# Performance work log

Hardware: AMD Instinct MI355X
Metric: run time of the kernel (lower is better)

Reference implementation:

```python
import jax, jax.numpy as jnp
import numpy as np

N, E, IN, ED, H, C, G, NC = 50000, 800000, 128, 32, 4, 16, 64, 2
HC = H * C  # 64
NEG_SLOPE = 0.2
EPS = 1e-5


def _layernorm(x, g, b):
    mu = jnp.mean(x, axis=-1, keepdims=True)
    var = jnp.mean((x - mu) ** 2, axis=-1, keepdims=True)
    return (x - mu) * jax.lax.rsqrt(var + EPS) * g + b


def _gat(x, src, dst, edge_attr, W, a_src, a_dst, We, a_edge, b):
    """PyG GATConv (v1) with edge features, concat=True."""
    n = x.shape[0]
    h, c = a_src.shape
    xw = (x @ W).reshape(n, h, c)                       # [N,H,C]
    al_src = jnp.sum(xw * a_src, axis=-1)               # [N,H]
    al_dst = jnp.sum(xw * a_dst, axis=-1)               # [N,H]
    ew = (edge_attr @ We).reshape(-1, h, c)             # [Ef,H,C]
    al_e = jnp.sum(ew * a_edge, axis=-1)                # [Ef,H]
    alpha = al_src[src] + al_dst[dst] + al_e            # [Ef,H]
    alpha = jnp.where(alpha > 0, alpha, NEG_SLOPE * alpha)
    # segment softmax over incoming edges of each dst node
    amax = jax.ops.segment_max(alpha, dst, num_segments=n)
    amax = jnp.where(jnp.isfinite(amax), amax, 0.0)
    ex = jnp.exp(alpha - amax[dst])
    denom = jax.ops.segment_sum(ex, dst, num_segments=n)
    att = ex / (denom[dst] + 1e-16)                     # [Ef,H]
    msg = xw[src] * att[:, :, None]                     # [Ef,H,C]
    out = jax.ops.segment_sum(msg, dst, num_segments=n) # [N,H,C]
    return out.reshape(n, h * c) + b


def setup_inputs() -> dict:
    ks = jax.random.split(jax.random.key(0), 24)
    s = 0.1
    inp = {
        "x": jax.random.normal(ks[0], (N, IN), jnp.float32),
        "edge_attr": jax.random.normal(ks[1], (E, ED), jnp.float32),
        "W1": jax.random.normal(ks[2], (IN, HC), jnp.float32) * s,
        "as1": jax.random.normal(ks[3], (H, C), jnp.float32) * s,
        "ad1": jax.random.normal(ks[4], (H, C), jnp.float32) * s,
        "We1": jax.random.normal(ks[5], (ED, HC), jnp.float32) * s,
        "ae1": jax.random.normal(ks[6], (H, C), jnp.float32) * s,
        "b1": jnp.zeros((HC,), jnp.float32),
        "W2": jax.random.normal(ks[7], (HC, HC), jnp.float32) * s,
        "as2": jax.random.normal(ks[8], (H, C), jnp.float32) * s,
        "ad2": jax.random.normal(ks[9], (H, C), jnp.float32) * s,
        "We2": jax.random.normal(ks[10], (ED, HC), jnp.float32) * s,
        "ae2": jax.random.normal(ks[11], (H, C), jnp.float32) * s,
        "b2": jnp.zeros((HC,), jnp.float32),
        "g1": jnp.ones((HC,), jnp.float32),
        "be1": jnp.zeros((HC,), jnp.float32),
        "fw1": jax.random.normal(ks[12], (HC, 32), jnp.float32) * s,
        "fb1": jnp.zeros((32,), jnp.float32),
        "g2": jnp.ones((32,), jnp.float32),
        "be2": jnp.zeros((32,), jnp.float32),
        "fw2": jax.random.normal(ks[13], (32, NC), jnp.float32) * s,
        "fb2": jnp.zeros((NC,), jnp.float32),
        "edge_index": jax.random.randint(ks[14], (2, E), 0, N, jnp.int64),
        "batch": jnp.sort(jax.random.randint(ks[15], (N,), 0, G, jnp.int64)),
    }
    return inp


def reference(x, edge_attr, W1, as1, ad1, We1, ae1, b1, W2, as2, ad2, We2, ae2,
              b2, g1, be1, fw1, fb1, g2, be2, fw2, fb2, edge_index, batch):
    src, dst = edge_index[0], edge_index[1]
    e = edge_attr.shape[0]
    # add_self_loops with fill_value='mean' (mean of incoming edge_attr per node)
    cnt = jax.ops.segment_sum(jnp.ones((e,), x.dtype), dst, num_segments=N)
    loop_ea = jax.ops.segment_sum(edge_attr, dst, num_segments=N) / jnp.clip(cnt, 1.0)[:, None]
    ar = jnp.arange(N)
    src_f = jnp.concatenate([src, ar])
    dst_f = jnp.concatenate([dst, ar])
    ea_f = jnp.concatenate([edge_attr, loop_ea], axis=0)

    h = _gat(x, src_f, dst_f, ea_f, W1, as1, ad1, We1, ae1, b1)
    h = jax.nn.relu(h)
    h = _layernorm(h, g1, be1)
    h = _gat(h, src_f, dst_f, ea_f, W2, as2, ad2, We2, ae2, b2)
    h = jax.nn.relu(h)
    pooled = jax.ops.segment_max(h, batch, num_segments=G)   # global_max_pool
    pooled = jnp.where(jnp.isfinite(pooled), pooled, 0.0)
    z = pooled @ fw1 + fb1
    z = _layernorm(z, g2, be2)
    z = jax.nn.relu(z)
    # dropout(p=0.4) is identity in eval mode
    z = z @ fw2 + fb2
    return jax.nn.log_softmax(z, axis=1)
```

## Files before the change

kernel.cpp:

```cpp
#include <hip/hip_runtime.h>
#include <math.h>

#define N_NODES 50000
#define N_EDGES 800000
#define IN_DIM 128
#define ED_DIM 32
#define NH 4
#define CH 16
#define HC 64
#define NG 64
#define NCL 2
#define NEG_SLOPE 0.2f
#define LN_EPS 1e-5f
#define NBLK1 196

__global__ void k_hist(const int* __restrict__ dst, int* __restrict__ cnt,
                       int* __restrict__ rank_e) {
    int e = blockIdx.x * 256 + threadIdx.x;
    if (e < N_EDGES) rank_e[e] = atomicAdd(&cnt[dst[e]], 1);
}

__global__ void k_scan_local(const int* __restrict__ cnt, int* __restrict__ tmp_ex,
                             int* __restrict__ bsum) {
    __shared__ int sd[256];
    int t = threadIdx.x, idx = blockIdx.x * 256 + t;
    int v = (idx < N_NODES) ? cnt[idx] : 0;
    sd[t] = v; __syncthreads();
    for (int off = 1; off < 256; off <<= 1) {
        int add = (t >= off) ? sd[t - off] : 0;
        __syncthreads();
        sd[t] += add;
        __syncthreads();
    }
    if (idx < N_NODES) tmp_ex[idx] = sd[t] - v;
    if (t == 255) bsum[blockIdx.x] = sd[t];
}

__global__ void k_scan_final(const int* __restrict__ tmp_ex, const int* __restrict__ bsum,
                             int* __restrict__ row_start) {
    __shared__ int sd[256];
    int t = threadIdx.x;
    int v = (t < NBLK1) ? bsum[t] : 0;
    sd[t] = v; __syncthreads();
    for (int off = 1; off < 256; off <<= 1) {
        int add = (t >= off) ? sd[t - off] : 0;
        __syncthreads();
        sd[t] += add;
        __syncthreads();
    }
    int boff = sd[blockIdx.x] - bsum[blockIdx.x];
    int idx = blockIdx.x * 256 + t;
    if (idx < N_NODES) row_start[idx] = tmp_ex[idx] + boff;
    if (idx == 0) row_start[N_NODES] = N_EDGES;
}

__global__ void k_edge_fused(const float* __restrict__ ea,
                             const float* __restrict__ We1, const float* __restrict__ ae1,
                             const float* __restrict__ We2, const float* __restrict__ ae2,
                             const int* __restrict__ dstI, const int* __restrict__ srcI,
                             const int* __restrict__ rank_e, const int* __restrict__ row_start,
                             float4* __restrict__ ale1, float4* __restrict__ ale2,
                             int* __restrict__ src_csr) {
    __shared__ float sVe[ED_DIM * 8];
    int t = threadIdx.x;
    {
        int d = t >> 3, k = t & 7;
        int l = k >> 2, h = k & 3;
        const float* We = l ? We2 : We1;
        const float* ae = l ? ae2 : ae1;
        float s = 0.f;
        #pragma unroll
        for (int c = 0; c < CH; ++c) s += We[d * HC + h * CH + c] * ae[h * CH + c];
        sVe[d * 8 + k] = s;
    }
    __syncthreads();
    int e = blockIdx.x * 256 + t;
    if (e >= N_EDGES) return;
    float a[8];
    #pragma unroll
    for (int k = 0; k < 8; ++k) a[k] = 0.f;
    const float4* er4 = (const float4*)(ea + (long long)e * ED_DIM);
    #pragma unroll
    for (int q = 0; q < ED_DIM / 4; ++q) {
        float4 v = er4[q];
        float ev[4] = {v.x, v.y, v.z, v.w};
        #pragma unroll
        for (int u = 0; u < 4; ++u) {
            #pragma unroll
            for (int k = 0; k < 8; ++k) a[k] += ev[u] * sVe[(q * 4 + u) * 8 + k];
        }
    }
    int pos = row_start[dstI[e]] + rank_e[e];
    src_csr[pos] = srcI[e];
    ale1[pos] = make_float4(a[0], a[1], a[2], a[3]);
    ale2[pos] = make_float4(a[4], a[5], a[6], a[7]);
}

template<int K>
__global__ void k_xw(const float* __restrict__ X, const float* __restrict__ W,
                     const float* __restrict__ AS, const float* __restrict__ AD,
                     float* __restrict__ XW, float* __restrict__ ALS, float* __restrict__ ALD) {
    __shared__ float sW[K * HC];
    __shared__ float sX[16 * K];
    int t = threadIdx.x;
    for (int i = t; i < K * HC; i += 256) sW[i] = W[i];
    int nb = blockIdx.x * 16;
    for (int i = t; i < 16 * K; i += 256) sX[i] = X[(long long)nb * K + i];
    __syncthreads();
    int sub = t >> 6, j = t & 63;
    float acc[4] = {0.f, 0.f, 0.f, 0.f};
    #pragma unroll 8
    for (int k = 0; k < K; ++k) {
        float wv = sW[k * HC + j];
        #pragma unroll
        for (int q = 0; q < 4; ++q) acc[q] += sX[(sub + 4 * q) * K + k] * wv;
    }
    float as_ = AS[j], ad_ = AD[j];
    #pragma unroll
    for (int q = 0; q < 4; ++q) {
        int n = nb + sub + 4 * q;
        XW[(long long)n * HC + j] = acc[q];
        float vs = acc[q] * as_, vd = acc[q] * ad_;
        #pragma unroll
        for (int m = 1; m < 16; m <<= 1) { vs += __shfl_xor(vs, m); vd += __shfl_xor(vd, m); }
        if ((j & 15) == 0) {
            int h = j >> 4;
            ALS[n * 4 + h] = vs; ALD[n * 4 + h] = vd;
        }
    }
}

template<bool DO_LN>
__global__ void k_agg(const int* __restrict__ rs, const int* __restrict__ srcs,
                      const float* __restrict__ ale,
                      const float* __restrict__ ALS, const float* __restrict__ ALD,
                      const float* __restrict__ XW, const float* __restrict__ bias,
                      const float* __restrict__ gam, const float* __restrict__ bet,
                      float* __restrict__ OUT) {
    int n = (blockIdx.x * blockDim.x + threadIdx.x) >> 6;
    if (n >= N_NODES) return;
    int lane = threadIdx.x & 63;
    int h = lane >> 4;
    int e0 = rs[n], e1 = rs[n + 1];
    float adn = ALD[n * 4 + h];
    float acc0 = 0.f, l0 = 0.f, as0 = 0.f;
    float acc1 = 0.f, l1 = 0.f, as1 = 0.f;
    float acc2 = 0.f, l2 = 0.f, as2 = 0.f;
    float acc3 = 0.f, l3 = 0.f, as3 = 0.f;
    int e = e0;
    for (; e + 3 < e1; e += 4) {
        int sA = srcs[e], sB = srcs[e + 1], sC = srcs[e + 2], sD = srcs[e + 3];
        float aeA = ale[(e) * 4 + h];
        float aeB = ale[(e + 1) * 4 + h];
        float aeC = ale[(e + 2) * 4 + h];
        float aeD = ale[(e + 3) * 4 + h];
        float xA = XW[sA * HC + lane];
        float xB = XW[sB * HC + lane];
        float xC = XW[sC * HC + lane];
        float xD = XW[sD * HC + lane];
        float aA = ALS[sA * 4 + h] + adn + aeA;
        float aB = ALS[sB * 4 + h] + adn + aeB;
        float aC = ALS[sC * 4 + h] + adn + aeC;
        float aD = ALS[sD * 4 + h] + adn + aeD;
        aA = aA > 0.f ? aA : NEG_SLOPE * aA;
        aB = aB > 0.f ? aB : NEG_SLOPE * aB;
        aC = aC > 0.f ? aC : NEG_SLOPE * aC;
        aD = aD > 0.f ? aD : NEG_SLOPE * aD;
        float qA = __expf(aA), qB = __expf(aB), qC = __expf(aC), qD = __expf(aD);
        acc0 += qA * xA; l0 += qA; as0 += aeA;
        acc1 += qB * xB; l1 += qB; as1 += aeB;
        acc2 += qC * xC; l2 += qC; as2 += aeC;
        acc3 += qD * xD; l3 += qD; as3 += aeD;
    }
    for (; e < e1; ++e) {
        int sA = srcs[e];
        float aeA = ale[(e) * 4 + h];
        float xA = XW[sA * HC + lane];
        float aA = ALS[sA * 4 + h] + adn + aeA;
        aA = aA > 0.f ? aA : NEG_SLOPE * aA;
        float qA = __expf(aA);
        acc0 += qA * xA; l0 += qA; as0 += aeA;
    }
    int d = e1 - e0;
    float invd = 1.f / (float)(d > 0 ? d : 1);
    float aSelf = ALS[n * 4 + h] + adn + (as0 + as1 + as2 + as3) * invd;
    aSelf = aSelf > 0.f ? aSelf : NEG_SLOPE * aSelf;
    float pS = __expf(aSelf);
    float acc = (acc0 + acc1) + (acc2 + acc3) + pS * XW[n * HC + lane];
    float l = (l0 + l1) + (l2 + l3) + pS;
    float v = acc / (l + 1e-16f) + bias[lane];
    v = fmaxf(v, 0.f);
    if (DO_LN) {
        float s1 = v;
        #pragma unroll
        for (int mm = 1; mm < 64; mm <<= 1) s1 += __shfl_xor(s1, mm);
        float mean = s1 * (1.f / 64.f);
        float dd = v - mean;
        float s2 = dd * dd;
        #pragma unroll
        for (int mm = 1; mm < 64; mm <<= 1) s2 += __shfl_xor(s2, mm);
        float var = s2 * (1.f / 64.f);
        v = dd * rsqrtf(var + LN_EPS) * gam[lane] + bet[lane];
    }
    OUT[(long long)n * HC + lane] = v;
}

__global__ void k_pool(const float* __restrict__ H2, const int* __restrict__ batch,
                       float* __restrict__ pooled) {
    int j = threadIdx.x & 63;
    int r = threadIdx.x >> 6;
    int base = blockIdx.x * 128;
    int gcur = -1; float rm = 0.f;
    for (int n = base + r; n < base + 128 && n < N_NODES; n += 4) {
        int g = batch[n];
        if (g != gcur) {
            if (gcur >= 0) atomicMax((unsigned int*)&pooled[gcur * HC + j], __float_as_uint(rm));
            gcur = g; rm = 0.f;
        }
        rm = fmaxf(rm, H2[(long long)n * HC + j]);
    }
    if (gcur >= 0) atomicMax((unsigned int*)&pooled[gcur * HC + j], __float_as_uint(rm));
}

__global__ void k_head(const float* __restrict__ pooled,
                       const float* __restrict__ fw1, const float* __restrict__ fb1,
                       const float* __restrict__ g2, const float* __restrict__ be2,
                       const float* __restrict__ fw2, const float* __restrict__ fb2,
                       float* __restrict__ out) {
    int g = blockIdx.x;
    int j = threadIdx.x;
    float z = 0.f;
    if (j < 32) {
        for (int k = 0; k < HC; ++k) z += pooled[g * HC + k] * fw1[k * 32 + j];
        z += fb1[j];
    }
    float s1 = (j < 32) ? z : 0.f;
    for (int m = 1; m < 32; m <<= 1) s1 += __shfl_xor(s1, m, 32);
    float mean = s1 * (1.f / 32.f);
    float d = z - mean;
    float s2 = (j < 32) ? d * d : 0.f;
    for (int m = 1; m < 32; m <<= 1) s2 += __shfl_xor(s2, m, 32);
    float var = s2 * (1.f / 32.f);
    float zz = 0.f;
    if (j < 32) {
        zz = d * rsqrtf(var + LN_EPS) * g2[j] + be2[j];
        zz = fmaxf(zz, 0.f);
    }
    float p0 = (j < 32) ? zz * fw2[j * NCL + 0] : 0.f;
    float p1 = (j < 32) ? zz * fw2[j * NCL + 1] : 0.f;
    for (int m = 1; m < 32; m <<= 1) { p0 += __shfl_xor(p0, m, 32); p1 += __shfl_xor(p1, m, 32); }
    if (j == 0) {
        float l0 = p0 + fb2[0], l1 = p1 + fb2[1];
        float mx = fmaxf(l0, l1);
        float ls = mx + logf(__expf(l0 - mx) + __expf(l1 - mx));
        out[g * NCL + 0] = l0 - ls;
        out[g * NCL + 1] = l1 - ls;
    }
}

extern "C" void kernel_launch(void* const* d_in, const int* in_sizes, int n_in,
                              void* d_out, int out_size, void* d_ws, size_t ws_size,
                              hipStream_t stream) {
    const float* x   = (const float*)d_in[0];
    const float* ea  = (const float*)d_in[1];
    const float* W1  = (const float*)d_in[2];
    const float* as1 = (const float*)d_in[3];
    const float* ad1 = (const float*)d_in[4];
    const float* We1 = (const float*)d_in[5];
    const float* ae1 = (const float*)d_in[6];
    const float* b1  = (const float*)d_in[7];
    const float* W2  = (const float*)d_in[8];
    const float* as2 = (const float*)d_in[9];
    const float* ad2 = (const float*)d_in[10];
    const float* We2 = (const float*)d_in[11];
    const float* ae2 = (const float*)d_in[12];
    const float* b2  = (const float*)d_in[13];
    const float* g1  = (const float*)d_in[14];
    const float* be1 = (const float*)d_in[15];
    const float* fw1 = (const float*)d_in[16];
    const float* fb1 = (const float*)d_in[17];
    const float* g2  = (const float*)d_in[18];
    const float* be2 = (const float*)d_in[19];
    const float* fw2 = (const float*)d_in[20];
    const float* fb2 = (const float*)d_in[21];
    const int* eidx  = (const int*)d_in[22];
    const int* batch = (const int*)d_in[23];
    const int* srcI = eidx;
    const int* dstI = eidx + N_EDGES;

    char* w = (char*)d_ws;
    auto alloc = [&](size_t bytes) { char* p = w; w += (bytes + 255) & ~(size_t)255; return p; };
    int*   cnt       = (int*)  alloc((size_t)N_NODES * 4);
    int*   row_start = (int*)  alloc((size_t)(N_NODES + 1) * 4);
    int*   rank_e    = (int*)  alloc((size_t)N_EDGES * 4);
    int*   tmp_ex    = (int*)  alloc((size_t)N_NODES * 4);
    int*   bsum      = (int*)  alloc(256 * 4);
    int*   src_csr   = (int*)  alloc((size_t)N_EDGES * 4);
    float4* ale1     = (float4*)alloc((size_t)N_EDGES * 16);
    float4* ale2     = (float4*)alloc((size_t)N_EDGES * 16);
    float* xw1       = (float*)alloc((size_t)N_NODES * HC * 4);
    float* als1      = (float*)alloc((size_t)N_NODES * 4 * 4);
    float* ald1      = (float*)alloc((size_t)N_NODES * 4 * 4);
    float* h1        = (float*)alloc((size_t)N_NODES * HC * 4);
    float* als2      = (float*)alloc((size_t)N_NODES * 4 * 4);
    float* ald2      = (float*)alloc((size_t)N_NODES * 4 * 4);
    float* pooled    = (float*)alloc((size_t)NG * HC * 4);
    float* xw2 = xw1;
    float* h2  = h1;

    hipMemsetAsync(cnt, 0, (size_t)N_NODES * 4, stream);
    hipMemsetAsync(pooled, 0, (size_t)NG * HC * 4, stream);

    k_hist<<<N_EDGES / 256, 256, 0, stream>>>(dstI, cnt, rank_e);
    k_scan_local<<<NBLK1, 256, 0, stream>>>(cnt, tmp_ex, bsum);
    k_scan_final<<<NBLK1, 256, 0, stream>>>(tmp_ex, bsum, row_start);
    k_edge_fused<<<N_EDGES / 256, 256, 0, stream>>>(ea, We1, ae1, We2, ae2, dstI, srcI,
                                                    rank_e, row_start, ale1, ale2, src_csr);

    k_xw<IN_DIM><<<N_NODES / 16, 256, 0, stream>>>(x, W1, as1, ad1, xw1, als1, ald1);
    k_agg<true><<<N_NODES / 4, 256, 0, stream>>>(row_start, src_csr, (const float*)ale1,
                                                 als1, ald1, xw1, b1, g1, be1, h1);
    k_xw<HC><<<N_NODES / 16, 256, 0, stream>>>(h1, W2, as2, ad2, xw2, als2, ald2);
    k_agg<false><<<N_NODES / 4, 256, 0, stream>>>(row_start, src_csr, (const float*)ale2,
                                                  als2, ald2, xw2, b2, nullptr, nullptr, h2);

    k_pool<<<(N_NODES + 127) / 128, 256, 0, stream>>>(h2, batch, pooled);
    k_head<<<NG, 64, 0, stream>>>(pooled, fw1, fb1, g2, be2, fw2, fb2, (float*)d_out);
}
```

Measured before the change: 465.1 us.

## Write edge attention logits in edge order and gather via CSR permutation

The edge-logit kernel now writes its eight per-edge logits contiguously in original edge order instead of scattering them into CSR positions. A separate permutation kernel writes (edge id, src) pairs into CSR order. The aggregation kernels then gather the logit through that permutation. This replaces scattered 16-byte writes with coalesced writes, at the cost of an extra launch and a random gather of the logit inside both aggregation passes.

```diff
diff --git a/kernel.cpp b/kernel.cpp
--- a/kernel.cpp
+++ b/kernel.cpp
@@ -54,13 +54,10 @@
     if (idx == 0) row_start[N_NODES] = N_EDGES;
 }
 
-__global__ void k_edge_fused(const float* __restrict__ ea,
-                             const float* __restrict__ We1, const float* __restrict__ ae1,
-                             const float* __restrict__ We2, const float* __restrict__ ae2,
-                             const int* __restrict__ dstI, const int* __restrict__ srcI,
-                             const int* __restrict__ rank_e, const int* __restrict__ row_start,
-                             float4* __restrict__ ale1, float4* __restrict__ ale2,
-                             int* __restrict__ src_csr) {
+__global__ void k_edge_lin(const float* __restrict__ ea,
+                           const float* __restrict__ We1, const float* __restrict__ ae1,
+                           const float* __restrict__ We2, const float* __restrict__ ae2,
+                           float4* __restrict__ ale8) {
     __shared__ float sVe[ED_DIM * 8];
     int t = threadIdx.x;
     {
@@ -90,10 +87,18 @@
             for (int k = 0; k < 8; ++k) a[k] += ev[u] * sVe[(q * 4 + u) * 8 + k];
         }
     }
-    int pos = row_start[dstI[e]] + rank_e[e];
-    src_csr[pos] = srcI[e];
-    ale1[pos] = make_float4(a[0], a[1], a[2], a[3]);
-    ale2[pos] = make_float4(a[4], a[5], a[6], a[7]);
+    float4* out = ale8 + (long long)e * 2;
+    out[0] = make_float4(a[0], a[1], a[2], a[3]);
+    out[1] = make_float4(a[4], a[5], a[6], a[7]);
+}
+
+__global__ void k_perm2(const int* __restrict__ dst, const int* __restrict__ srcI,
+                        const int* __restrict__ rank_e, const int* __restrict__ row_start,
+                        int2* __restrict__ perm_src) {
+    int e = blockIdx.x * 256 + threadIdx.x;
+    if (e >= N_EDGES) return;
+    int pos = row_start[dst[e]] + rank_e[e];
+    perm_src[pos] = make_int2(e, srcI[e]);
 }
 
 template<int K>
@@ -130,9 +135,9 @@
     }
 }
 
-template<bool DO_LN>
-__global__ void k_agg(const int* __restrict__ rs, const int* __restrict__ srcs,
-                      const float* __restrict__ ale,
+template<bool DO_LN, int LOFF>
+__global__ void k_agg(const int* __restrict__ rs, const int2* __restrict__ ps,
+                      const float* __restrict__ ale8,
                       const float* __restrict__ ALS, const float* __restrict__ ALD,
                       const float* __restrict__ XW, const float* __restrict__ bias,
                       const float* __restrict__ gam, const float* __restrict__ bet,
@@ -149,19 +154,19 @@
     float acc3 = 0.f, l3 = 0.f, as3 = 0.f;
     int e = e0;
     for (; e + 3 < e1; e += 4) {
-        int sA = srcs[e], sB = srcs[e + 1], sC = srcs[e + 2], sD = srcs[e + 3];
-        float aeA = ale[(e) * 4 + h];
-        float aeB = ale[(e + 1) * 4 + h];
-        float aeC = ale[(e + 2) * 4 + h];
-        float aeD = ale[(e + 3) * 4 + h];
-        float xA = XW[sA * HC + lane];
-        float xB = XW[sB * HC + lane];
-        float xC = XW[sC * HC + lane];
-        float xD = XW[sD * HC + lane];
-        float aA = ALS[sA * 4 + h] + adn + aeA;
-        float aB = ALS[sB * 4 + h] + adn + aeB;
-        float aC = ALS[sC * 4 + h] + adn + aeC;
-        float aD = ALS[sD * 4 + h] + adn + aeD;
+        int2 pA = ps[e], pB = ps[e + 1], pC = ps[e + 2], pD = ps[e + 3];
+        float aeA = ale8[(long long)pA.x * 8 + LOFF + h];
+        float aeB = ale8[(long long)pB.x * 8 + LOFF + h];
+        float aeC = ale8[(long long)pC.x * 8 + LOFF + h];
+        float aeD = ale8[(long long)pD.x * 8 + LOFF + h];
+        float xA = XW[pA.y * HC + lane];
+        float xB = XW[pB.y * HC + lane];
+        float xC = XW[pC.y * HC + lane];
+        float xD = XW[pD.y * HC + lane];
+        float aA = ALS[pA.y * 4 + h] + adn + aeA;
+        float aB = ALS[pB.y * 4 + h] + adn + aeB;
+        float aC = ALS[pC.y * 4 + h] + adn + aeC;
+        float aD = ALS[pD.y * 4 + h] + adn + aeD;
         aA = aA > 0.f ? aA : NEG_SLOPE * aA;
         aB = aB > 0.f ? aB : NEG_SLOPE * aB;
         aC = aC > 0.f ? aC : NEG_SLOPE * aC;
@@ -173,10 +178,10 @@
         acc3 += qD * xD; l3 += qD; as3 += aeD;
     }
     for (; e < e1; ++e) {
-        int sA = srcs[e];
-        float aeA = ale[(e) * 4 + h];
-        float xA = XW[sA * HC + lane];
-        float aA = ALS[sA * 4 + h] + adn + aeA;
+        int2 pA = ps[e];
+        float aeA = ale8[(long long)pA.x * 8 + LOFF + h];
+        float xA = XW[pA.y * HC + lane];
+        float aA = ALS[pA.y * 4 + h] + adn + aeA;
         aA = aA > 0.f ? aA : NEG_SLOPE * aA;
         float qA = __expf(aA);
         acc0 += qA * xA; l0 += qA; as0 += aeA;
@@ -295,9 +300,8 @@
     int*   rank_e    = (int*)  alloc((size_t)N_EDGES * 4);
     int*   tmp_ex    = (int*)  alloc((size_t)N_NODES * 4);
     int*   bsum      = (int*)  alloc(256 * 4);
-    int*   src_csr   = (int*)  alloc((size_t)N_EDGES * 4);
-    float4* ale1     = (float4*)alloc((size_t)N_EDGES * 16);
-    float4* ale2     = (float4*)alloc((size_t)N_EDGES * 16);
+    int2*  perm_src  = (int2*) alloc((size_t)N_EDGES * 8);
+    float4* ale8     = (float4*)alloc((size_t)N_EDGES * 32);
     float* xw1       = (float*)alloc((size_t)N_NODES * HC * 4);
     float* als1      = (float*)alloc((size_t)N_NODES * 4 * 4);
     float* ald1      = (float*)alloc((size_t)N_NODES * 4 * 4);
@@ -314,15 +318,15 @@
     k_hist<<<N_EDGES / 256, 256, 0, stream>>>(dstI, cnt, rank_e);
     k_scan_local<<<NBLK1, 256, 0, stream>>>(cnt, tmp_ex, bsum);
     k_scan_final<<<NBLK1, 256, 0, stream>>>(tmp_ex, bsum, row_start);
-    k_edge_fused<<<N_EDGES / 256, 256, 0, stream>>>(ea, We1, ae1, We2, ae2, dstI, srcI,
-                                                    rank_e, row_start, ale1, ale2, src_csr);
+    k_edge_lin<<<N_EDGES / 256, 256, 0, stream>>>(ea, We1, ae1, We2, ae2, ale8);
+    k_perm2<<<N_EDGES / 256, 256, 0, stream>>>(dstI, srcI, rank_e, row_start, perm_src);
 
     k_xw<IN_DIM><<<N_NODES / 16, 256, 0, stream>>>(x, W1, as1, ad1, xw1, als1, ald1);
-    k_agg<true><<<N_NODES / 4, 256, 0, stream>>>(row_start, src_csr, (const float*)ale1,
-                                                 als1, ald1, xw1, b1, g1, be1, h1);
+    k_agg<true, 0><<<N_NODES / 4, 256, 0, stream>>>(row_start, perm_src, (const float*)ale8,
+                                                    als1, ald1, xw1, b1, g1, be1, h1);
     k_xw<HC><<<N_NODES / 16, 256, 0, stream>>>(h1, W2, as2, ad2, xw2, als2, ald2);
-    k_agg<false><<<N_NODES / 4, 256, 0, stream>>>(row_start, src_csr, (const float*)ale2,
-                                                  als2, ald2, xw2, b2, nullptr, nullptr, h2);
+    k_agg<false, 4><<<N_NODES / 4, 256, 0, stream>>>(row_start, perm_src, (const float*)ale8,
+                                                     als2, ald2, xw2, b2, nullptr, nullptr, h2);
 
     k_pool<<<(N_NODES + 127) / 128, 256, 0, stream>>>(h2, batch, pooled);
     k_head<<<NG, 64, 0, stream>>>(pooled, fw1, fb1, g2, be2, fw2, fb2, (float*)d_out);
```

New measurement: 458.4 us. Within noise of the previous version (-1.4%).
